# Optimization experiments

Hardware: AMD Instinct MI355X
Metric: run time of the kernel (lower is better)

Reference implementation:

```python
import jax, jax.numpy as jnp
import numpy as np

B, S, DM, H, D = 2, 2048, 1024, 16, 64

def setup_inputs() -> dict:
    key = jax.random.key(0)
    ks = jax.random.split(key, 9)
    def g(k, shape, scale=0.02):
        return jax.random.normal(k, shape, dtype=jnp.float32) * scale
    return {
        "x":  jax.random.normal(ks[0], (B, S, DM), dtype=jnp.float32),
        "Wq": g(ks[1], (DM, H * D)), "bq": g(ks[2], (H * D,)),
        "Wk": g(ks[3], (DM, H * D)), "bk": g(ks[4], (H * D,)),
        "Wv": g(ks[5], (DM, H * D)), "bv": g(ks[6], (H * D,)),
        "Wo": g(ks[7], (H * D, DM)), "bo": g(ks[8], (DM,)),
    }

def reference(x, Wq, bq, Wk, bk, Wv, bv, Wo, bo):
    b, s, _ = x.shape
    # projections -> (B, H, S, D)
    q = (x @ Wq + bq).reshape(b, s, H, D).transpose(0, 2, 1, 3)
    k = (x @ Wk + bk).reshape(b, s, H, D).transpose(0, 2, 1, 3)
    v = (x @ Wv + bv).reshape(b, s, H, D).transpose(0, 2, 1, 3)
    # naive attention: full (B,H,S,S) scores, causal mask, softmax
    scores = jnp.einsum("bhqd,bhkd->bhqk", q, k) / jnp.sqrt(jnp.float32(D))
    causal = jnp.tril(jnp.ones((s, s), dtype=bool))
    scores = jnp.where(causal[None, None], scores, jnp.float32(-jnp.inf))
    weights = jax.nn.softmax(scores, axis=-1)
    out = jnp.einsum("bhqk,bhkd->bhqd", weights, v)  # (B,H,S,D)
    out = out.transpose(0, 2, 1, 3).reshape(b, s, H * D)
    return out @ Wo + bo  # dropout_p = 0 -> identity
```

## Files before the change

### kernel.cpp

```cpp
#include <hip/hip_runtime.h>
#include <hip/hip_bf16.h>

typedef __hip_bfloat16 bf16;
typedef __attribute__((ext_vector_type(8))) short bf16x8;
typedef __attribute__((ext_vector_type(4))) float f32x4;
typedef __attribute__((ext_vector_type(4))) unsigned int u32x4;

#define MFMA_BF16(a, b, c) __builtin_amdgcn_mfma_f32_16x16x32_bf16((a), (b), (c), 0, 0, 0)

static constexpr int B_  = 2;
static constexpr int S_  = 2048;
static constexpr int DM_ = 1024;
static constexpr int H_  = 16;
static constexpr int D_  = 64;
static constexpr int M_  = B_ * S_;

__device__ __forceinline__ void load16(const void* g, void* l) {
  __builtin_amdgcn_global_load_lds(
      (const __attribute__((address_space(1))) void*)g,
      (__attribute__((address_space(3))) void*)l, 16, 0, 0);
}

__device__ __forceinline__ unsigned int pack_bf16(float lo, float hi) {
  const unsigned int ul = __builtin_bit_cast(unsigned short, __float2bfloat16(lo));
  const unsigned int uh = __builtin_bit_cast(unsigned short, __float2bfloat16(hi));
  return (uh << 16) | ul;
}


__global__ void cvt_f32_bf16_kernel(const float* __restrict__ in,
                                    bf16* __restrict__ out, int n4) {
  int i = blockIdx.x * blockDim.x + threadIdx.x;
  if (i >= n4) return;
  float4 v = ((const float4*)in)[i];
  ushort4 u;
  u.x = __builtin_bit_cast(unsigned short, __float2bfloat16(v.x));
  u.y = __builtin_bit_cast(unsigned short, __float2bfloat16(v.y));
  u.z = __builtin_bit_cast(unsigned short, __float2bfloat16(v.z));
  u.w = __builtin_bit_cast(unsigned short, __float2bfloat16(v.w));
  ((ushort4*)out)[i] = u;
}

__global__ void transpose_cvt_kernel(const float* __restrict__ w0,
                                     const float* __restrict__ w1,
                                     const float* __restrict__ w2,
                                     const float* __restrict__ w3,
                                     bf16* __restrict__ o0, bf16* __restrict__ o1,
                                     bf16* __restrict__ o2, bf16* __restrict__ o3) {
  __shared__ float t[32][33];
  const float* in = blockIdx.z == 0 ? w0 : blockIdx.z == 1 ? w1 : blockIdx.z == 2 ? w2 : w3;
  bf16* out = blockIdx.z == 0 ? o0 : blockIdx.z == 1 ? o1 : blockIdx.z == 2 ? o2 : o3;
  int tx = threadIdx.x & 31;
  int ty = threadIdx.x >> 5;
  int r0 = blockIdx.y * 32;
  int c0 = blockIdx.x * 32;
#pragma unroll
  for (int yy = 0; yy < 32; yy += 8)
    t[ty + yy][tx] = in[(size_t)(r0 + ty + yy) * DM_ + c0 + tx];
  __syncthreads();
#pragma unroll
  for (int yy = 0; yy < 32; yy += 8)
    out[(size_t)(c0 + ty + yy) * DM_ + r0 + tx] = __float2bfloat16(t[tx][ty + yy]);
}

template <int MODE>
__global__ __launch_bounds__(256) void gemm_bt_kernel(
    const bf16* __restrict__ A, const bf16* __restrict__ Bt,
    const float* __restrict__ bias, const float* __restrict__ bias2,
    const float* __restrict__ bias3, void* __restrict__ out, int K) {
  __shared__ bf16 As[2][128 * 32];
  __shared__ bf16 Bs[2][128 * 32];
  const int tid = threadIdx.x;
  const int wid = tid >> 6, lane = tid & 63;
  const int g = lane >> 4, c = lane & 15;
  const int wr = wid >> 1, wc = wid & 1;
  const int bm = blockIdx.x, bn = blockIdx.y;

  f32x4 acc[4][4] = {};

  const char* Ag = (const char*)(A + (size_t)bm * 128 * K);
  const char* Bg = (const char*)(Bt + (size_t)bn * 128 * K);
  const int f0 = tid * 16, f1 = f0 + 4096;
  const int r0 = f0 >> 6, cb0 = f0 & 63;
  const int r1 = f1 >> 6;
  const size_t rowbytes = (size_t)K * 2;

  auto stage = [&](int kt, int bufi) {
    const size_t koff = (size_t)kt * 64;
    load16(Ag + (size_t)r0 * rowbytes + koff + cb0, (char*)As[bufi] + f0);
    load16(Ag + (size_t)r1 * rowbytes + koff + cb0, (char*)As[bufi] + f1);
    load16(Bg + (size_t)r0 * rowbytes + koff + cb0, (char*)Bs[bufi] + f0);
    load16(Bg + (size_t)r1 * rowbytes + koff + cb0, (char*)Bs[bufi] + f1);
  };

  const int NT = K / 32;
  stage(0, 0);
  int cur = 0;
#pragma unroll 1
  for (int kt = 0; kt < NT; ++kt) {
    if (kt + 1 < NT) {
      stage(kt + 1, cur ^ 1);
      asm volatile("s_waitcnt vmcnt(4)" ::: "memory");
    } else {
      asm volatile("s_waitcnt vmcnt(0)" ::: "memory");
    }
    __builtin_amdgcn_s_barrier();

    bf16x8 af[4], bfr[4];
#pragma unroll
    for (int mi = 0; mi < 4; ++mi)
      af[mi] = *(const bf16x8*)&As[cur][(wr * 64 + mi * 16 + c) * 32 + g * 8];
#pragma unroll
    for (int ni = 0; ni < 4; ++ni)
      bfr[ni] = *(const bf16x8*)&Bs[cur][(wc * 64 + ni * 16 + c) * 32 + g * 8];
    __builtin_amdgcn_s_setprio(1);
#pragma unroll
    for (int mi = 0; mi < 4; ++mi)
#pragma unroll
      for (int ni = 0; ni < 4; ++ni)
        acc[mi][ni] = MFMA_BF16(af[mi], bfr[ni], acc[mi][ni]);
    __builtin_amdgcn_s_setprio(0);

    if (kt + 1 < NT) __builtin_amdgcn_s_barrier();
    cur ^= 1;
  }

#pragma unroll
  for (int ni = 0; ni < 4; ++ni) {
    const int n_g = bn * 128 + wc * 64 + ni * 16 + c;
    float bv;
    if constexpr (MODE == 3) {
      const int proj = n_g >> 10, ncol = n_g & 1023;
      bv = proj == 0 ? bias[ncol] : proj == 1 ? bias2[ncol] : bias3[ncol];
    } else {
      bv = bias[n_g];
    }
#pragma unroll
    for (int mi = 0; mi < 4; ++mi) {
#pragma unroll
      for (int r = 0; r < 4; ++r) {
        const int m_g = bm * 128 + wr * 64 + mi * 16 + g * 4 + r;
        const float val = acc[mi][ni][r] + bv;
        if constexpr (MODE == 2) {
          ((float*)out)[(size_t)m_g * DM_ + n_g] = val;
        } else {
          const int proj = n_g >> 10, ncol = n_g & 1023;
          const int b = m_g >> 11, s = m_g & (S_ - 1);
          const int h = ncol >> 6, d = ncol & (D_ - 1);
          size_t idx = (size_t)proj * 4194304;
          if (proj < 2)
            idx += (((size_t)(b * H_ + h)) * S_ + s) * D_ + d;
          else
            idx += (((size_t)(b * H_ + h)) * D_ + d) * S_ + s;
          ((bf16*)out)[idx] = __float2bfloat16(val);
        }
      }
    }
  }
}

__global__ __launch_bounds__(256, 4) void flash_attn_kernel(
    const bf16* __restrict__ Q, const bf16* __restrict__ Kg,
    const bf16* __restrict__ Vt, bf16* __restrict__ Aout) {
  __shared__ bf16 Ks[2][64 * 64];
  __shared__ bf16 Vs[2][64 * 64];
  const int tid = threadIdx.x;
  const int w = tid >> 6, lane = tid & 63;
  const int g = lane >> 4, c = lane & 15;

  const int bid = blockIdx.x;
  const int xcd = bid & 7, loc = bid >> 3;
  const int bh = xcd * 4 + (loc & 3);
  const int j = 31 - (loc >> 2);
  const int t = j * 4 + w;
  const int b = bh >> 4, h = bh & (H_ - 1);

  const float ALPHA2 = 0.125f * 1.44269504f;
  const float THR2 = 11.5f;
  const float NEG_INF = -__builtin_inff();

  const char* Kbase = (const char*)(Kg + (size_t)bh * S_ * D_);
  const char* Vbase = (const char*)(Vt + (size_t)bh * D_ * S_);
  const int s0 = tid, s1 = tid + 256;
  const int sr0 = s0 >> 3, sq0 = ((s0 & 7) ^ (sr0 & 7)) << 4;
  const int sr1 = s1 >> 3, sq1 = ((s1 & 7) ^ (sr1 & 7)) << 4;

  const bf16* Qp = Q + ((size_t)bh * S_ + t * 16 + c) * D_;
  bf16x8 qf[2];
  qf[0] = *(const bf16x8*)&Qp[g * 8];
  qf[1] = *(const bf16x8*)&Qp[32 + g * 8];

  bf16x8 onesf;
#pragma unroll
  for (int jj = 0; jj < 8; ++jj) onesf[jj] = (short)0x3f80;

  f32x4 o[4] = {};
  f32x4 lacc = {};
  float m = -1000.0f;

  const int rowlim = w * 16 + c;
  const int src0 = ((g & 1) * 2) * 16 + c;
  const int src1 = src0 + 16;
  const bool ghi = (g >= 2);
  const int cs = c & 7;
  int roff[2][4];
#pragma unroll
  for (int kk = 0; kk < 2; ++kk)
#pragma unroll
    for (int n = 0; n < 4; ++n)
      roff[kk][n] = n * 2048 + c * 128 + (((kk * 4 + g) ^ cs) << 4);

  {
    load16(Kbase + sr0 * 128 + sq0, (char*)Ks[0] + s0 * 16);
    load16(Kbase + sr1 * 128 + sq1, (char*)Ks[0] + s1 * 16);
    load16(Vbase + sr0 * 4096 + sq0, (char*)Vs[0] + s0 * 16);
    load16(Vbase + sr1 * 4096 + sq1, (char*)Vs[0] + s1 * 16);
  }
  __syncthreads();

  int cur = 0;
#pragma unroll 1
  for (int kv = 0; kv <= j; ++kv) {
    if (kv < j) {
      const char* Krow = Kbase + (size_t)(kv + 1) * 8192;
      const char* Vcol = Vbase + (size_t)(kv + 1) * 128;
      const int nb = cur ^ 1;
      load16(Krow + sr0 * 128 + sq0, (char*)Ks[nb] + s0 * 16);
      load16(Krow + sr1 * 128 + sq1, (char*)Ks[nb] + s1 * 16);
      load16(Vcol + sr0 * 4096 + sq0, (char*)Vs[nb] + s0 * 16);
      load16(Vcol + sr1 * 4096 + sq1, (char*)Vs[nb] + s1 * 16);
    }

    const char* Kt = (const char*)Ks[cur];
    const char* Vtile = (const char*)Vs[cur];
    bf16x8 kf[2][4];
#pragma unroll
    for (int kk = 0; kk < 2; ++kk)
#pragma unroll
      for (int n = 0; n < 4; ++n)
        kf[kk][n] = *(const bf16x8*)(Kt + roff[kk][n]);

    f32x4 st[4] = {};
    __builtin_amdgcn_s_setprio(1);
#pragma unroll
    for (int n = 0; n < 4; ++n) {
      st[n] = MFMA_BF16(kf[0][n], qf[0], st[n]);
      st[n] = MFMA_BF16(kf[1][n], qf[1], st[n]);
    }
    __builtin_amdgcn_s_setprio(0);

    bf16x8 vf[2][4];
#pragma unroll
    for (int kk = 0; kk < 2; ++kk)
#pragma unroll
      for (int n = 0; n < 4; ++n)
        vf[kk][n] = *(const bf16x8*)(Vtile + roff[kk][n]);

    float aa[4][4];
#pragma unroll
    for (int n = 0; n < 4; ++n)
#pragma unroll
      for (int r = 0; r < 4; ++r)
        aa[n][r] = fmaf(st[n][r], ALPHA2, -m);
    if (kv == j) {
#pragma unroll
      for (int n = 0; n < 4; ++n)
#pragma unroll
        for (int r = 0; r < 4; ++r)
          if (n * 16 + g * 4 + r > rowlim) aa[n][r] = NEG_INF;
    }

    float lm;
    {
      float t0 = fmaxf(fmaxf(aa[0][0], aa[0][1]), fmaxf(aa[0][2], aa[0][3]));
      float t1 = fmaxf(fmaxf(aa[1][0], aa[1][1]), fmaxf(aa[1][2], aa[1][3]));
      float t2 = fmaxf(fmaxf(aa[2][0], aa[2][1]), fmaxf(aa[2][2], aa[2][3]));
      float t3 = fmaxf(fmaxf(aa[3][0], aa[3][1]), fmaxf(aa[3][2], aa[3][3]));
      lm = fmaxf(fmaxf(t0, t1), fmaxf(t2, t3));
    }

    if (__any(lm > THR2)) {
      float dm = fmaxf(lm, __shfl_xor(lm, 16, 64));
      dm = fmaxf(dm, __shfl_xor(dm, 32, 64));
      const float sh = fmaxf(dm, 0.0f);
      const float sc = __builtin_amdgcn_exp2f(-sh);
      m += sh;
#pragma unroll
      for (int r = 0; r < 4; ++r) lacc[r] *= sc;
#pragma unroll
      for (int n = 0; n < 4; ++n)
#pragma unroll
        for (int r = 0; r < 4; ++r) o[n][r] *= sc;
#pragma unroll
      for (int n = 0; n < 4; ++n)
#pragma unroll
        for (int r = 0; r < 4; ++r) aa[n][r] -= sh;
    }

    float p[4][4];
#pragma unroll
    for (int n = 0; n < 4; ++n)
#pragma unroll
      for (int r = 0; r < 4; ++r) p[n][r] = __builtin_amdgcn_exp2f(aa[n][r]);

    unsigned int dw[4][2];
#pragma unroll
    for (int n = 0; n < 4; ++n) {
      dw[n][0] = pack_bf16(p[n][0], p[n][1]);
      dw[n][1] = pack_bf16(p[n][2], p[n][3]);
    }

#pragma unroll
    for (int kk = 0; kk < 2; ++kk) {
      unsigned int bb[4];
      {
        unsigned int lo = __shfl(dw[kk * 2][0], src0, 64);
        unsigned int hi = __shfl(dw[kk * 2 + 1][0], src0, 64);
        bb[0] = ghi ? hi : lo;
      }
      {
        unsigned int lo = __shfl(dw[kk * 2][1], src0, 64);
        unsigned int hi = __shfl(dw[kk * 2 + 1][1], src0, 64);
        bb[1] = ghi ? hi : lo;
      }
      {
        unsigned int lo = __shfl(dw[kk * 2][0], src1, 64);
        unsigned int hi = __shfl(dw[kk * 2 + 1][0], src1, 64);
        bb[2] = ghi ? hi : lo;
      }
      {
        unsigned int lo = __shfl(dw[kk * 2][1], src1, 64);
        unsigned int hi = __shfl(dw[kk * 2 + 1][1], src1, 64);
        bb[3] = ghi ? hi : lo;
      }
      u32x4 bbv = {bb[0], bb[1], bb[2], bb[3]};
      bf16x8 pb = __builtin_bit_cast(bf16x8, bbv);
      __builtin_amdgcn_s_setprio(1);
#pragma unroll
      for (int n = 0; n < 4; ++n) o[n] = MFMA_BF16(vf[kk][n], pb, o[n]);
      lacc = MFMA_BF16(onesf, pb, lacc);
      __builtin_amdgcn_s_setprio(0);
    }

    __syncthreads();
    cur ^= 1;
  }

  const float inv = 1.0f / lacc[0];

  bf16* Arow = Aout + ((size_t)b * S_ + t * 16 + c) * (H_ * D_) + h * D_;
#pragma unroll
  for (int n = 0; n < 4; ++n) {
    ushort4 u;
    u.x = __builtin_bit_cast(unsigned short, __float2bfloat16(o[n][0] * inv));
    u.y = __builtin_bit_cast(unsigned short, __float2bfloat16(o[n][1] * inv));
    u.z = __builtin_bit_cast(unsigned short, __float2bfloat16(o[n][2] * inv));
    u.w = __builtin_bit_cast(unsigned short, __float2bfloat16(o[n][3] * inv));
    *(ushort4*)&Arow[n * 16 + g * 4] = u;
  }
}


extern "C" void kernel_launch(void* const* d_in, const int* in_sizes, int n_in,
                              void* d_out, int out_size, void* d_ws, size_t ws_size,
                              hipStream_t stream) {
  (void)in_sizes; (void)n_in; (void)out_size; (void)ws_size;
  const float* x  = (const float*)d_in[0];
  const float* Wq = (const float*)d_in[1];
  const float* bq = (const float*)d_in[2];
  const float* Wk = (const float*)d_in[3];
  const float* bk = (const float*)d_in[4];
  const float* Wv = (const float*)d_in[5];
  const float* bv = (const float*)d_in[6];
  const float* Wo = (const float*)d_in[7];
  const float* bo = (const float*)d_in[8];
  float* out = (float*)d_out;

  char* ws = (char*)d_ws;
  bf16* xb  = (bf16*)(ws);
  bf16* Wqt = (bf16*)(ws + (8u << 20));
  bf16* Wkt = (bf16*)(ws + (10u << 20));
  bf16* Wvt = (bf16*)(ws + (12u << 20));
  bf16* Wot = (bf16*)(ws + (14u << 20));
  bf16* Qb  = (bf16*)(ws + (16u << 20));
  bf16* Kb  = (bf16*)(ws + (24u << 20));
  bf16* Vtb = (bf16*)(ws + (32u << 20));
  bf16* Ab  = xb;

  cvt_f32_bf16_kernel<<<4096, 256, 0, stream>>>(x, xb, (M_ * DM_) / 4);
  transpose_cvt_kernel<<<dim3(32, 32, 4), 256, 0, stream>>>(
      Wq, Wk, Wv, Wo, Wqt, Wkt, Wvt, Wot);

  gemm_bt_kernel<3><<<dim3(32, 24), 256, 0, stream>>>(
      xb, Wqt, bq, bk, bv, (void*)Qb, DM_);

  flash_attn_kernel<<<dim3(1024), 256, 0, stream>>>(Qb, Kb, Vtb, Ab);

  gemm_bt_kernel<2><<<dim3(32, 8), 256, 0, stream>>>(
      Ab, Wot, bo, nullptr, nullptr, (void*)out, DM_);
}
```

Measured before the change: 119.0 us.

## Merge prep kernels, shrink output GEMM tile, reorder attention block schedule

Folds the x conversion into the weight transpose kernel so one launch replaces two. Gives the output projection its own GEMM with 128x64 tiles, raising the grid from 256 to 512 blocks so more CUs are busy. Changes the causal flash-attention block order from strictly heaviest-first to an interleaved pattern meant to balance work across waves. Each piece adds some code complexity, and the smaller tile lowers per-block data reuse.

```diff
diff --git a/kernel.cpp b/kernel.cpp
--- a/kernel.cpp
+++ b/kernel.cpp
@@ -27,26 +27,29 @@
   return (uh << 16) | ul;
 }
 
-
-__global__ void cvt_f32_bf16_kernel(const float* __restrict__ in,
-                                    bf16* __restrict__ out, int n4) {
-  int i = blockIdx.x * blockDim.x + threadIdx.x;
-  if (i >= n4) return;
-  float4 v = ((const float4*)in)[i];
-  ushort4 u;
-  u.x = __builtin_bit_cast(unsigned short, __float2bfloat16(v.x));
-  u.y = __builtin_bit_cast(unsigned short, __float2bfloat16(v.y));
-  u.z = __builtin_bit_cast(unsigned short, __float2bfloat16(v.z));
-  u.w = __builtin_bit_cast(unsigned short, __float2bfloat16(v.w));
-  ((ushort4*)out)[i] = u;
-}
-
-__global__ void transpose_cvt_kernel(const float* __restrict__ w0,
-                                     const float* __restrict__ w1,
-                                     const float* __restrict__ w2,
-                                     const float* __restrict__ w3,
-                                     bf16* __restrict__ o0, bf16* __restrict__ o1,
-                                     bf16* __restrict__ o2, bf16* __restrict__ o3) {
+__global__ void prep_kernel(const float* __restrict__ w0,
+                            const float* __restrict__ w1,
+                            const float* __restrict__ w2,
+                            const float* __restrict__ w3,
+                            const float* __restrict__ x,
+                            bf16* __restrict__ o0, bf16* __restrict__ o1,
+                            bf16* __restrict__ o2, bf16* __restrict__ o3,
+                            bf16* __restrict__ xb) {
+  if (blockIdx.z == 4) {
+    const int blk = blockIdx.y * 32 + blockIdx.x;
+#pragma unroll
+    for (int rep = 0; rep < 4; ++rep) {
+      const int i = blk * 1024 + rep * 256 + threadIdx.x;
+      float4 v = ((const float4*)x)[i];
+      ushort4 u;
+      u.x = __builtin_bit_cast(unsigned short, __float2bfloat16(v.x));
+      u.y = __builtin_bit_cast(unsigned short, __float2bfloat16(v.y));
+      u.z = __builtin_bit_cast(unsigned short, __float2bfloat16(v.z));
+      u.w = __builtin_bit_cast(unsigned short, __float2bfloat16(v.w));
+      ((ushort4*)xb)[i] = u;
+    }
+    return;
+  }
   __shared__ float t[32][33];
   const float* in = blockIdx.z == 0 ? w0 : blockIdx.z == 1 ? w1 : blockIdx.z == 2 ? w2 : w3;
   bf16* out = blockIdx.z == 0 ? o0 : blockIdx.z == 1 ? o1 : blockIdx.z == 2 ? o2 : o3;
@@ -63,11 +66,10 @@
     out[(size_t)(c0 + ty + yy) * DM_ + r0 + tx] = __float2bfloat16(t[tx][ty + yy]);
 }
 
-template <int MODE>
-__global__ __launch_bounds__(256) void gemm_bt_kernel(
+__global__ __launch_bounds__(256) void gemm_qkv_kernel(
     const bf16* __restrict__ A, const bf16* __restrict__ Bt,
     const float* __restrict__ bias, const float* __restrict__ bias2,
-    const float* __restrict__ bias3, void* __restrict__ out, int K) {
+    const float* __restrict__ bias3, bf16* __restrict__ out, int K) {
   __shared__ bf16 As[2][128 * 32];
   __shared__ bf16 Bs[2][128 * 32];
   const int tid = threadIdx.x;
@@ -128,32 +130,97 @@
 #pragma unroll
   for (int ni = 0; ni < 4; ++ni) {
     const int n_g = bn * 128 + wc * 64 + ni * 16 + c;
-    float bv;
-    if constexpr (MODE == 3) {
-      const int proj = n_g >> 10, ncol = n_g & 1023;
-      bv = proj == 0 ? bias[ncol] : proj == 1 ? bias2[ncol] : bias3[ncol];
-    } else {
-      bv = bias[n_g];
-    }
+    const int proj = n_g >> 10, ncol = n_g & 1023;
+    const float bv = proj == 0 ? bias[ncol] : proj == 1 ? bias2[ncol] : bias3[ncol];
+    const int h = ncol >> 6, d = ncol & (D_ - 1);
 #pragma unroll
     for (int mi = 0; mi < 4; ++mi) {
 #pragma unroll
       for (int r = 0; r < 4; ++r) {
         const int m_g = bm * 128 + wr * 64 + mi * 16 + g * 4 + r;
         const float val = acc[mi][ni][r] + bv;
-        if constexpr (MODE == 2) {
-          ((float*)out)[(size_t)m_g * DM_ + n_g] = val;
-        } else {
-          const int proj = n_g >> 10, ncol = n_g & 1023;
-          const int b = m_g >> 11, s = m_g & (S_ - 1);
-          const int h = ncol >> 6, d = ncol & (D_ - 1);
-          size_t idx = (size_t)proj * 4194304;
-          if (proj < 2)
-            idx += (((size_t)(b * H_ + h)) * S_ + s) * D_ + d;
-          else
-            idx += (((size_t)(b * H_ + h)) * D_ + d) * S_ + s;
-          ((bf16*)out)[idx] = __float2bfloat16(val);
-        }
+        const int b = m_g >> 11, s = m_g & (S_ - 1);
+        size_t idx = (size_t)proj * 4194304;
+        if (proj < 2)
+          idx += (((size_t)(b * H_ + h)) * S_ + s) * D_ + d;
+        else
+          idx += (((size_t)(b * H_ + h)) * D_ + d) * S_ + s;
+        out[idx] = __float2bfloat16(val);
+      }
+    }
+  }
+}
+
+__global__ __launch_bounds__(256) void gemm_out_kernel(
+    const bf16* __restrict__ A, const bf16* __restrict__ Bt,
+    const float* __restrict__ bias, float* __restrict__ out, int K) {
+  __shared__ bf16 As[2][128 * 32];
+  __shared__ bf16 Bs[2][64 * 32];
+  const int tid = threadIdx.x;
+  const int wid = tid >> 6, lane = tid & 63;
+  const int g = lane >> 4, c = lane & 15;
+  const int wr = wid >> 1, wc = wid & 1;
+  const int bm = blockIdx.x, bn = blockIdx.y;
+
+  f32x4 acc[4][2] = {};
+
+  const char* Ag = (const char*)(A + (size_t)bm * 128 * K);
+  const char* Bg = (const char*)(Bt + (size_t)bn * 64 * K);
+  const int s0 = tid, s1 = tid + 256;
+  const int ra0 = s0 >> 2, ca0 = (s0 & 3) * 16;
+  const int ra1 = s1 >> 2, ca1 = (s1 & 3) * 16;
+  const int rb = tid >> 2, cb2 = (tid & 3) * 16;
+  const size_t rowbytes = (size_t)K * 2;
+
+  auto stage = [&](int kt, int bufi) {
+    const size_t koff = (size_t)kt * 64;
+    load16(Ag + (size_t)ra0 * rowbytes + koff + ca0, (char*)As[bufi] + s0 * 16);
+    load16(Ag + (size_t)ra1 * rowbytes + koff + ca1, (char*)As[bufi] + s1 * 16);
+    load16(Bg + (size_t)rb * rowbytes + koff + cb2, (char*)Bs[bufi] + tid * 16);
+  };
+
+  const int NT = K / 32;
+  stage(0, 0);
+  int cur = 0;
+#pragma unroll 1
+  for (int kt = 0; kt < NT; ++kt) {
+    if (kt + 1 < NT) {
+      stage(kt + 1, cur ^ 1);
+      asm volatile("s_waitcnt vmcnt(3)" ::: "memory");
+    } else {
+      asm volatile("s_waitcnt vmcnt(0)" ::: "memory");
+    }
+    __builtin_amdgcn_s_barrier();
+
+    bf16x8 af[4], bfr[2];
+#pragma unroll
+    for (int mi = 0; mi < 4; ++mi)
+      af[mi] = *(const bf16x8*)&As[cur][(wr * 64 + mi * 16 + c) * 32 + g * 8];
+#pragma unroll
+    for (int ni = 0; ni < 2; ++ni)
+      bfr[ni] = *(const bf16x8*)&Bs[cur][(wc * 32 + ni * 16 + c) * 32 + g * 8];
+    __builtin_amdgcn_s_setprio(1);
+#pragma unroll
+    for (int mi = 0; mi < 4; ++mi)
+#pragma unroll
+      for (int ni = 0; ni < 2; ++ni)
+        acc[mi][ni] = MFMA_BF16(af[mi], bfr[ni], acc[mi][ni]);
+    __builtin_amdgcn_s_setprio(0);
+
+    if (kt + 1 < NT) __builtin_amdgcn_s_barrier();
+    cur ^= 1;
+  }
+
+#pragma unroll
+  for (int ni = 0; ni < 2; ++ni) {
+    const int n_g = bn * 64 + wc * 32 + ni * 16 + c;
+    const float bv = bias[n_g];
+#pragma unroll
+    for (int mi = 0; mi < 4; ++mi) {
+#pragma unroll
+      for (int r = 0; r < 4; ++r) {
+        const int m_g = bm * 128 + wr * 64 + mi * 16 + g * 4 + r;
+        out[(size_t)m_g * DM_ + n_g] = acc[mi][ni][r] + bv;
       }
     }
   }
@@ -171,7 +238,10 @@
   const int bid = blockIdx.x;
   const int xcd = bid & 7, loc = bid >> 3;
   const int bh = xcd * 4 + (loc & 3);
-  const int j = 31 - (loc >> 2);
+  const int u = loc >> 2;
+  const int slot = u >> 3, q = u & 7;
+  const int j = slot == 0 ? 31 - q : slot == 1 ? 16 + q
+              : slot == 2 ? 15 - q : q;
   const int t = j * 4 + w;
   const int b = bh >> 4, h = bh & (H_ - 1);
 
@@ -351,12 +421,12 @@
   bf16* Arow = Aout + ((size_t)b * S_ + t * 16 + c) * (H_ * D_) + h * D_;
 #pragma unroll
   for (int n = 0; n < 4; ++n) {
-    ushort4 u;
-    u.x = __builtin_bit_cast(unsigned short, __float2bfloat16(o[n][0] * inv));
-    u.y = __builtin_bit_cast(unsigned short, __float2bfloat16(o[n][1] * inv));
-    u.z = __builtin_bit_cast(unsigned short, __float2bfloat16(o[n][2] * inv));
-    u.w = __builtin_bit_cast(unsigned short, __float2bfloat16(o[n][3] * inv));
-    *(ushort4*)&Arow[n * 16 + g * 4] = u;
+    ushort4 u2;
+    u2.x = __builtin_bit_cast(unsigned short, __float2bfloat16(o[n][0] * inv));
+    u2.y = __builtin_bit_cast(unsigned short, __float2bfloat16(o[n][1] * inv));
+    u2.z = __builtin_bit_cast(unsigned short, __float2bfloat16(o[n][2] * inv));
+    u2.w = __builtin_bit_cast(unsigned short, __float2bfloat16(o[n][3] * inv));
+    *(ushort4*)&Arow[n * 16 + g * 4] = u2;
   }
 }
 
@@ -387,15 +457,13 @@
   bf16* Vtb = (bf16*)(ws + (32u << 20));
   bf16* Ab  = xb;
 
-  cvt_f32_bf16_kernel<<<4096, 256, 0, stream>>>(x, xb, (M_ * DM_) / 4);
-  transpose_cvt_kernel<<<dim3(32, 32, 4), 256, 0, stream>>>(
-      Wq, Wk, Wv, Wo, Wqt, Wkt, Wvt, Wot);
-
-  gemm_bt_kernel<3><<<dim3(32, 24), 256, 0, stream>>>(
-      xb, Wqt, bq, bk, bv, (void*)Qb, DM_);
+  prep_kernel<<<dim3(32, 32, 5), 256, 0, stream>>>(
+      Wq, Wk, Wv, Wo, x, Wqt, Wkt, Wvt, Wot, xb);
+
+  gemm_qkv_kernel<<<dim3(32, 24), 256, 0, stream>>>(
+      xb, Wqt, bq, bk, bv, Qb, DM_);
 
   flash_attn_kernel<<<dim3(1024), 256, 0, stream>>>(Qb, Kb, Vtb, Ab);
 
-  gemm_bt_kernel<2><<<dim3(32, 8), 256, 0, stream>>>(
-      Ab, Wot, bo, nullptr, nullptr, (void*)out, DM_);
-}
+  gemm_out_kernel<<<dim3(32, 16), 256, 0, stream>>>(Ab, Wot, bo, out, DM_);
+}
```

New measurement: 113.2 us (median of 2 runs). 1.05x faster.
